# Performance work log

Hardware: AMD Instinct MI355X
Metric: run time of the kernel (lower is better)

## Reference

```python
import jax, jax.numpy as jnp
import numpy as np

B = 8192
TEXT_DIM = 2048
GRAPH_DIM = 1024
OUT_DIM = 1024
C = 2048  # common_dim = max(text_dim, graph_dim)
H = 16    # num_heads
LN_EPS = 1e-5


def _linear(x, W, b):
    # torch nn.Linear: y = x @ W.T + b, W: [out, in]
    return x @ W.T + b


def _mha(q, k, v, Wqkv, bqkv, Wo, bo):
    # Faithful to torch nn.MultiheadAttention (batch_first, eval mode).
    # Wqkv: [3C, C], bqkv: [3C], Wo: [C, C], bo: [C]
    Bq, S, _ = q.shape
    D = C // H
    Wq, Wk, Wv = Wqkv[:C], Wqkv[C:2 * C], Wqkv[2 * C:]
    bq, bk, bv = bqkv[:C], bqkv[C:2 * C], bqkv[2 * C:]
    qh = _linear(q, Wq, bq).reshape(Bq, S, H, D).transpose(0, 2, 1, 3)  # [B,H,S,D]
    kh = _linear(k, Wk, bk).reshape(Bq, S, H, D).transpose(0, 2, 1, 3)
    vh = _linear(v, Wv, bv).reshape(Bq, S, H, D).transpose(0, 2, 1, 3)
    scores = jnp.einsum('bhqd,bhkd->bhqk', qh, kh) / jnp.sqrt(jnp.asarray(D, qh.dtype))
    attn = jax.nn.softmax(scores, axis=-1)
    out = jnp.einsum('bhqk,bhkd->bhqd', attn, vh)
    out = out.transpose(0, 2, 1, 3).reshape(Bq, S, C)
    return _linear(out, Wo, bo)


def _layernorm(x, w, b):
    mu = jnp.mean(x, axis=-1, keepdims=True)
    var = jnp.mean(jnp.square(x - mu), axis=-1, keepdims=True)
    return (x - mu) * jax.lax.rsqrt(var + LN_EPS) * w + b


def setup_inputs() -> dict:
    key = jax.random.key(0)
    ks = jax.random.split(key, 16)
    s = 0.02
    return {
        'text_embeddings': jax.random.normal(ks[0], (B, TEXT_DIM), jnp.float32),
        'graph_embeddings': jax.random.normal(ks[1], (B, GRAPH_DIM), jnp.float32),
        'Wt': jax.random.normal(ks[2], (C, TEXT_DIM), jnp.float32) * s,
        'bt': jnp.zeros((C,), jnp.float32),
        'Wg': jax.random.normal(ks[3], (C, GRAPH_DIM), jnp.float32) * s,
        'bg': jnp.zeros((C,), jnp.float32),
        'Wqkv_s': jax.random.normal(ks[4], (3 * C, C), jnp.float32) * s,
        'bqkv_s': jnp.zeros((3 * C,), jnp.float32),
        'Wo_s': jax.random.normal(ks[5], (C, C), jnp.float32) * s,
        'bo_s': jnp.zeros((C,), jnp.float32),
        'Wqkv_c': jax.random.normal(ks[6], (3 * C, C), jnp.float32) * s,
        'bqkv_c': jnp.zeros((3 * C,), jnp.float32),
        'Wo_c': jax.random.normal(ks[7], (C, C), jnp.float32) * s,
        'bo_c': jnp.zeros((C,), jnp.float32),
        'ln_w': jnp.ones((C,), jnp.float32),
        'ln_b': jnp.zeros((C,), jnp.float32),
        'Wout': jax.random.normal(ks[8], (OUT_DIM, C), jnp.float32) * s,
        'bout': jnp.zeros((OUT_DIM,), jnp.float32),
    }


def reference(text_embeddings, graph_embeddings, Wt, bt, Wg, bg,
              Wqkv_s, bqkv_s, Wo_s, bo_s, Wqkv_c, bqkv_c, Wo_c, bo_c,
              ln_w, ln_b, Wout, bout):
    text_proj = _linear(text_embeddings, Wt, bt)    # [B, C]
    graph_proj = _linear(graph_embeddings, Wg, bg)  # [B, C]
    stacked = jnp.stack([text_proj, graph_proj], axis=1)  # [B, 2, C]
    attn_out = _mha(stacked, stacked, stacked, Wqkv_s, bqkv_s, Wo_s, bo_s)
    attn_out = _layernorm(attn_out, ln_w, ln_b)
    cross = _mha(attn_out, stacked, stacked, Wqkv_c, bqkv_c, Wo_c, bo_c)
    attn_out = attn_out + cross
    fused = jnp.mean(attn_out, axis=1)  # [B, C]
    return _linear(fused, Wout, bout)   # [B, OUT_DIM]
```

## Files before the change

### kernel.cpp

```cpp
#include <hip/hip_runtime.h>
#include <cstdio>

typedef unsigned short u16;
typedef float f32x4 __attribute__((ext_vector_type(4)));
typedef short s16x8 __attribute__((ext_vector_type(8)));

__device__ __forceinline__ u16 f2bf(float x) {
    unsigned u = __float_as_uint(x);
    u += 0x7fffu + ((u >> 16) & 1u);
    return (u16)(u >> 16);
}
__device__ __forceinline__ unsigned pack2(float a, float b) {
    return (unsigned)f2bf(a) | ((unsigned)f2bf(b) << 16);
}
__device__ __forceinline__ void unpack2(unsigned u, float& lo, float& hi) {
    lo = __uint_as_float(u << 16);
    hi = __uint_as_float(u & 0xffff0000u);
}

__device__ __forceinline__ void gl2lds16(const u16* g, u16* l) {
    __builtin_amdgcn_global_load_lds(
        (const __attribute__((address_space(1))) void*)g,
        (__attribute__((address_space(3))) void*)l, 16, 0, 0);
}

__global__ __launch_bounds__(256) void cast_w7(
    const float* __restrict__ p0, const float* __restrict__ p1,
    const float* __restrict__ p2, const float* __restrict__ p3,
    const float* __restrict__ p4, const float* __restrict__ p5,
    const float* __restrict__ p6, u16* __restrict__ dst) {
    long i = (long)blockIdx.x * 256 + threadIdx.x;
    if (i >= 10485760L) return;
    const float* src;
    long base;
    if (i < 3145728L)      { src = p0; base = 0L; }
    else if (i < 6291456L) { src = p1; base = 3145728L; }
    else if (i < 7340032L) { src = p2; base = 6291456L; }
    else if (i < 8388608L) { src = p3; base = 7340032L; }
    else if (i < 9437184L) { src = p4; base = 8388608L; }
    else if (i < 9961472L) { src = p5; base = 9437184L; }
    else                   { src = p6; base = 9961472L; }
    float4 v = ((const float4*)src)[i - base];
    uint2 r;
    r.x = pack2(v.x, v.y);
    r.y = pack2(v.z, v.w);
    ((uint2*)dst)[i] = r;
}

__global__ __launch_bounds__(256) void cast_in(const float* __restrict__ t,
                                               const float* __restrict__ g,
                                               u16* __restrict__ yt,
                                               u16* __restrict__ yg,
                                               int nt4, int ng4) {
    int i = blockIdx.x * 256 + threadIdx.x;
    const float* src;
    u16* dst;
    int idx;
    if (i < nt4) {
        src = t; dst = yt; idx = i;
    } else {
        idx = i - nt4;
        if (idx >= ng4) return;
        src = g; dst = yg;
    }
    float4 v = ((const float4*)src)[idx];
    uint2 r;
    r.x = pack2(v.x, v.y);
    r.y = pack2(v.z, v.w);
    ((uint2*)dst)[idx] = r;
}

template <bool OUT_BF16>
__global__ __launch_bounds__(256) void gemm_async(const u16* __restrict__ A, int lda,
                                                  const u16* __restrict__ B,
                                                  const float* __restrict__ bias,
                                                  void* __restrict__ Cout,
                                                  int K, int ldc) {
    __shared__ __align__(16) u16 As[128 * 32];
    __shared__ __align__(16) u16 Bs[128 * 32];

    const int tid = threadIdx.x;
    const int lane = tid & 63;
    const int wave = tid >> 6;
    const int wm = wave >> 1;
    const int wn = wave & 1;
    const size_t bm = (size_t)blockIdx.y * 128;
    const size_t bn = (size_t)blockIdx.x * 128;

    f32x4 acc[4][4];
#pragma unroll
    for (int i = 0; i < 4; ++i)
#pragma unroll
        for (int j = 0; j < 4; ++j) acc[i][j] = (f32x4)0.f;

    const int srow = tid >> 2;
    const int scol = (tid & 3) << 3;
    const u16* Ag = A + (bm + (size_t)srow) * (size_t)lda + scol;
    const u16* Bg = B + (bn + (size_t)srow) * (size_t)K + scol;
    const size_t rA = (size_t)64 * lda;
    const size_t rB = (size_t)64 * K;
    u16* lA0 = &As[tid * 8];
    u16* lA1 = &As[2048 + tid * 8];
    u16* lB0 = &Bs[tid * 8];
    u16* lB1 = &Bs[2048 + tid * 8];

    const int lrow = lane & 15;
    const int lk = (lane >> 4) << 3;

    const int niter = K >> 5;
    for (int t = 0; t < niter; ++t) {
        __syncthreads();
        gl2lds16(Ag, lA0);
        gl2lds16(Ag + rA, lA1);
        gl2lds16(Bg, lB0);
        gl2lds16(Bg + rB, lB1);
        Ag += 32;
        Bg += 32;
        __syncthreads();
        s16x8 af[4], bfr[4];
#pragma unroll
        for (int i = 0; i < 4; ++i)
            af[i] = *(const s16x8*)&As[(wm * 64 + i * 16 + lrow) * 32 + lk];
#pragma unroll
        for (int j = 0; j < 4; ++j)
            bfr[j] = *(const s16x8*)&Bs[(wn * 64 + j * 16 + lrow) * 32 + lk];
#pragma unroll
        for (int i = 0; i < 4; ++i)
#pragma unroll
            for (int j = 0; j < 4; ++j)
                acc[i][j] = __builtin_amdgcn_mfma_f32_16x16x32_bf16(
                    af[i], bfr[j], acc[i][j], 0, 0, 0);
    }

    const size_t crow0 = bm + wm * 64 + ((lane >> 4) << 2);
    const int ccol0 = (int)bn + wn * 64 + (lane & 15);
#pragma unroll
    for (int i = 0; i < 4; ++i) {
#pragma unroll
        for (int j = 0; j < 4; ++j) {
            const int col = ccol0 + j * 16;
            const float bv = bias[col];
            const size_t base = (crow0 + (size_t)i * 16) * (size_t)ldc + col;
#pragma unroll
            for (int r = 0; r < 4; ++r) {
                const float v = acc[i][j][r] + bv;
                if (OUT_BF16)
                    ((u16*)Cout)[base + (size_t)r * ldc] = f2bf(v);
                else
                    ((float*)Cout)[base + (size_t)r * ldc] = v;
            }
        }
    }
}

#define STG_A02(v)                                                            \
    do {                                                                      \
        gl2lds16(aG + (size_t)(v) * 64, &As[(v) & 1][tid * 8]);               \
        gl2lds16(aG + 2 * a64 + (size_t)(v) * 64,                             \
                 &As[(v) & 1][8192 + tid * 8]);                               \
    } while (0)
#define STG_A13(v)                                                            \
    do {                                                                      \
        gl2lds16(aG + a64 + (size_t)(v) * 64, &As[(v) & 1][4096 + tid * 8]);  \
        gl2lds16(aG + 3 * a64 + (size_t)(v) * 64,                             \
                 &As[(v) & 1][12288 + tid * 8]);                              \
    } while (0)
#define STG_B01(v)                                                            \
    do {                                                                      \
        gl2lds16(bG + (size_t)(v) * 64, &Bs[(v) & 1][tid * 8]);               \
        gl2lds16(bG + b64 + (size_t)(v) * 64, &Bs[(v) & 1][4096 + tid * 8]);  \
    } while (0)
#define STG_B23(v)                                                            \
    do {                                                                      \
        gl2lds16(bG + 2 * b64 + (size_t)(v) * 64,                             \
                 &Bs[(v) & 1][8192 + tid * 8]);                               \
        gl2lds16(bG + 3 * b64 + (size_t)(v) * 64,                             \
                 &Bs[(v) & 1][12288 + tid * 8]);                              \
    } while (0)
#define RD_AF(buf, mh, m)                                                     \
    do {                                                                      \
        const u16* p_ = &As[buf][aRow + ((mh) * 64 + (m) * 16) * 64];         \
        aF[m][0] = *(const s16x8*)(p_ + aK0);                                 \
        aF[m][1] = *(const s16x8*)(p_ + aK1);                                 \
    } while (0)
#define RD_B(buf, nh, dst)                                                    \
    do {                                                                      \
        _Pragma("unroll") for (int n_ = 0; n_ < 2; ++n_) {                    \
            const u16* p_ = &Bs[buf][bRow + ((nh) * 32 + n_ * 16) * 64];      \
            dst[n_][0] = *(const s16x8*)(p_ + aK0);                           \
            dst[n_][1] = *(const s16x8*)(p_ + aK1);                           \
        }                                                                     \
    } while (0)
#define MFMA4(ar, bv, ci, cj)                                                 \
    do {                                                                      \
        acc[ci][cj] = __builtin_amdgcn_mfma_f32_16x16x32_bf16(                \
            (ar)[0], (bv)[0], acc[ci][cj], 0, 0, 0);                          \
        acc[ci][cj] = __builtin_amdgcn_mfma_f32_16x16x32_bf16(                \
            (ar)[1], (bv)[1], acc[ci][cj], 0, 0, 0);                          \
    } while (0)

#define TILEW(u, SA13, S2, RDN, V2S, V4S)                                     \
    do {                                                                      \
        const int cur = (u) & 1, oth = cur ^ 1;                               \
                                                          \
        if (SA13) STG_A13((u) + 1);                                           \
        RD_B(cur, 1, b1);                                                     \
        __builtin_amdgcn_s_setprio(1);                                        \
        _Pragma("unroll") for (int m = 0; m < 4; ++m) {                       \
            MFMA4(aF[m], b0[0], m, 0);                                        \
            MFMA4(aF[m], b0[1], m, 1);                                        \
        }                                                                     \
        __builtin_amdgcn_s_setprio(0);                                        \
        asm volatile("s_waitcnt " V2S ::: "memory");                          \
        __builtin_amdgcn_s_barrier();                                         \
                                  \
        if (S2) STG_A02((u) + 2);                                             \
        __builtin_amdgcn_s_setprio(1);                                        \
        _Pragma("unroll") for (int m = 0; m < 4; ++m) {                       \
            MFMA4(aF[m], b1[0], m, 2);                                        \
            MFMA4(aF[m], b1[1], m, 3);                                        \
            RD_AF(cur, 1, m);                                                 \
        }                                                                     \
        __builtin_amdgcn_s_setprio(0);                                        \
        __builtin_amdgcn_s_barrier();                                         \
                                                          \
        if (S2) STG_B01((u) + 2);                                             \
        __builtin_amdgcn_s_setprio(1);                                        \
        _Pragma("unroll") for (int m = 0; m < 4; ++m) {                       \
            MFMA4(aF[m], b1[0], 4 + m, 2);                                    \
            MFMA4(aF[m], b1[1], 4 + m, 3);                                    \
        }                                                                     \
        __builtin_amdgcn_s_setprio(0);                                        \
        asm volatile("s_waitcnt " V4S ::: "memory");                          \
        __builtin_amdgcn_s_barrier();                                         \
                         \
        if (S2) STG_B23((u) + 2);                                             \
        __builtin_amdgcn_s_setprio(1);                                        \
        _Pragma("unroll") for (int m = 0; m < 4; ++m) {                       \
            MFMA4(aF[m], b0[0], 4 + m, 0);                                    \
            MFMA4(aF[m], b0[1], 4 + m, 1);                                    \
            if (RDN) RD_AF(oth, 0, m);                                        \
        }                                                                     \
        __builtin_amdgcn_s_setprio(0);                                        \
        if (RDN) RD_B(oth, 0, b0);                                            \
        __builtin_amdgcn_s_barrier();                                         \
    } while (0)

template <bool OUT_BF16>
__global__ __launch_bounds__(512, 2) void gemm8(const u16* __restrict__ A, int lda,
                                                const u16* __restrict__ B,
                                                const float* __restrict__ bias,
                                                void* __restrict__ Cout,
                                                int K, int ldc) {
    __shared__ __align__(16) u16 As[2][16384];
    __shared__ __align__(16) u16 Bs[2][16384];

    const int tid = threadIdx.x;
    const int lane = tid & 63;
    const int wave = tid >> 6;
    const int wm = wave >> 2;
    const int wn = wave & 3;

    const unsigned nwg = gridDim.x * gridDim.y;
    const unsigned orig = blockIdx.y * gridDim.x + blockIdx.x;
    const unsigned q = nwg >> 3, r = nwg & 7u;
    const unsigned xcd = orig & 7u, idx = orig >> 3;
    const unsigned wg =
        (xcd < r ? xcd * (q + 1) : r * (q + 1) + (xcd - r) * q) + idx;
    const size_t bm = (size_t)(wg / gridDim.x) * 256;
    const size_t bn = (size_t)(wg % gridDim.x) * 256;

    f32x4 acc[8][4];
#pragma unroll
    for (int i = 0; i < 8; ++i)
#pragma unroll
        for (int j = 0; j < 4; ++j) acc[i][j] = (f32x4)0.f;

    const int strow = tid >> 3;
    const int ssw = ((tid & 7) << 3) ^ ((strow & 7) << 3);
    const u16* aG = A + (bm + (size_t)strow) * (size_t)lda + ssw;
    const u16* bG = B + (bn + (size_t)strow) * (size_t)K + ssw;
    const size_t a64 = (size_t)64 * lda;
    const size_t b64 = (size_t)64 * K;

    const int lrow = lane & 15;
    const int hi8 = (lane >> 4) << 3;
    const int fswz = (lrow & 7) << 3;
    const int aK0 = hi8 ^ fswz;
    const int aK1 = (32 + hi8) ^ fswz;
    const int aRow = (wm * 128 + lrow) * 64;
    const int bRow = (wn * 64 + lrow) * 64;

    s16x8 aF[4][2], b0[2][2], b1[2][2];

    const int NT = K >> 6;

    STG_A02(0);
    STG_A13(0);
    STG_B01(0);
    STG_B23(0);
    STG_A02(1);
    STG_B01(1);
    STG_B23(1);
    asm volatile("s_waitcnt vmcnt(6)" ::: "memory");
    __builtin_amdgcn_s_barrier();
#pragma unroll
    for (int m = 0; m < 4; ++m) RD_AF(0, 0, m);
    RD_B(0, 0, b0);

    for (int u = 0; u < NT - 2; ++u)
        TILEW(u, 1, 1, 1, "vmcnt(8)", "vmcnt(6)");
    TILEW(NT - 2, 1, 0, 1, "vmcnt(8)", "vmcnt(2)");
    TILEW(NT - 1, 0, 0, 0, "vmcnt(0)", "vmcnt(0)");

    const size_t crow0 = bm + wm * 128 + ((lane >> 4) << 2);
    const int ccol0 = (int)bn + wn * 64 + (lane & 15);
#pragma unroll
    for (int im = 0; im < 8; ++im) {
#pragma unroll
        for (int in = 0; in < 4; ++in) {
            const int col = ccol0 + in * 16;
            const float bv = bias[col];
            const size_t base = (crow0 + (size_t)im * 16) * (size_t)ldc + col;
#pragma unroll
            for (int r = 0; r < 4; ++r) {
                const float v = acc[im][in][r] + bv;
                if (OUT_BF16)
                    ((u16*)Cout)[base + (size_t)r * ldc] = f2bf(v);
                else
                    ((float*)Cout)[base + (size_t)r * ldc] = v;
            }
        }
    }
}

#undef STG_A02
#undef STG_A13
#undef STG_B01
#undef STG_B23
#undef RD_AF
#undef RD_B
#undef MFMA4
#undef TILEW

__device__ __forceinline__ void dot8(uint4 a, uint4 b, float& acc) {
    const unsigned* pa = (const unsigned*)&a;
    const unsigned* pb = (const unsigned*)&b;
#pragma unroll
    for (int i = 0; i < 4; ++i) {
        float alo, ahi, blo, bhi;
        unpack2(pa[i], alo, ahi);
        unpack2(pb[i], blo, bhi);
        acc += alo * blo + ahi * bhi;
    }
}

__global__ __launch_bounds__(256) void attn2(u16* __restrict__ qkv) {
    const int b = (blockIdx.x * 256 + threadIdx.x) >> 6;
    const int l = threadIdx.x & 63;
    u16* t0 = qkv + (size_t)(2 * b) * 6144;
    u16* t1 = t0 + 6144;
    const float scale = 0.0883883476483184f;
#pragma unroll
    for (int hg = 0; hg < 4; ++hg) {
        const int o = hg * 512 + l * 8;
        const uint4 q0 = *(const uint4*)(t0 + o);
        const uint4 q1 = *(const uint4*)(t1 + o);
        const uint4 k0 = *(const uint4*)(t0 + 2048 + o);
        const uint4 k1 = *(const uint4*)(t1 + 2048 + o);
        float s00 = 0.f, s01 = 0.f, s10 = 0.f, s11 = 0.f;
        dot8(q0, k0, s00);
        dot8(q0, k1, s01);
        dot8(q1, k0, s10);
        dot8(q1, k1, s11);
#pragma unroll
        for (int m = 1; m < 16; m <<= 1) {
            s00 += __shfl_xor(s00, m);
            s01 += __shfl_xor(s01, m);
            s10 += __shfl_xor(s10, m);
            s11 += __shfl_xor(s11, m);
        }
        s00 *= scale; s01 *= scale; s10 *= scale; s11 *= scale;
        const float m0 = fmaxf(s00, s01), m1 = fmaxf(s10, s11);
        const float e00 = __expf(s00 - m0), e01 = __expf(s01 - m0);
        const float e10 = __expf(s10 - m1), e11 = __expf(s11 - m1);
        const float r0 = 1.f / (e00 + e01), r1 = 1.f / (e10 + e11);
        const float p00 = e00 * r0, p01 = e01 * r0;
        const float p10 = e10 * r1, p11 = e11 * r1;
        const uint4 v0 = *(const uint4*)(t0 + 4096 + o);
        const uint4 v1 = *(const uint4*)(t1 + 4096 + o);
        const unsigned* pv0 = (const unsigned*)&v0;
        const unsigned* pv1 = (const unsigned*)&v1;
        uint4 c0v, c1v;
        unsigned* pc0 = (unsigned*)&c0v;
        unsigned* pc1 = (unsigned*)&c1v;
#pragma unroll
        for (int i = 0; i < 4; ++i) {
            float alo, ahi, blo, bhi;
            unpack2(pv0[i], alo, ahi);
            unpack2(pv1[i], blo, bhi);
            pc0[i] = pack2(p00 * alo + p01 * blo, p00 * ahi + p01 * bhi);
            pc1[i] = pack2(p10 * alo + p11 * blo, p10 * ahi + p11 * bhi);
        }
        *(uint4*)(t0 + o) = c0v;
        *(uint4*)(t1 + o) = c1v;
    }
}

__global__ __launch_bounds__(256) void ln_k(const u16* __restrict__ x, int ldx,
                                            const float* __restrict__ w,
                                            const float* __restrict__ bb,
                                            u16* __restrict__ y) {
    __shared__ float red[8];
    const int row = blockIdx.x;
    const int tid = threadIdx.x;
    const uint4 v = ((const uint4*)(x + (size_t)row * ldx))[tid];
    const unsigned* pw = (const unsigned*)&v;
    float f[8];
#pragma unroll
    for (int i = 0; i < 4; ++i) unpack2(pw[i], f[2 * i], f[2 * i + 1]);
    float s = 0.f, q = 0.f;
#pragma unroll
    for (int i = 0; i < 8; ++i) {
        s += f[i];
        q += f[i] * f[i];
    }
#pragma unroll
    for (int off = 32; off > 0; off >>= 1) {
        s += __shfl_down(s, off);
        q += __shfl_down(q, off);
    }
    if ((tid & 63) == 0) {
        red[tid >> 6] = s;
        red[4 + (tid >> 6)] = q;
    }
    __syncthreads();
    s = red[0] + red[1] + red[2] + red[3];
    q = red[4] + red[5] + red[6] + red[7];
    const float mu = s * (1.f / 2048.f);
    const float var = q * (1.f / 2048.f) - mu * mu;
    const float rstd = rsqrtf(var + 1e-5f);
    const float4 w0 = ((const float4*)w)[2 * tid];
    const float4 w1 = ((const float4*)w)[2 * tid + 1];
    const float4 b0 = ((const float4*)bb)[2 * tid];
    const float4 b1 = ((const float4*)bb)[2 * tid + 1];
    const float wv[8] = {w0.x, w0.y, w0.z, w0.w, w1.x, w1.y, w1.z, w1.w};
    const float bv[8] = {b0.x, b0.y, b0.z, b0.w, b1.x, b1.y, b1.z, b1.w};
    uint4 o;
    unsigned* po = (unsigned*)&o;
#pragma unroll
    for (int i = 0; i < 4; ++i) {
        float lo = (f[2 * i] - mu) * rstd * wv[2 * i] + bv[2 * i];
        float hi = (f[2 * i + 1] - mu) * rstd * wv[2 * i + 1] + bv[2 * i + 1];
        po[i] = pack2(lo, hi);
    }
    ((uint4*)(y + (size_t)row * 2048))[tid] = o;
}

__global__ __launch_bounds__(256) void mean_res(const u16* __restrict__ ln,
                                                const u16* __restrict__ co,
                                                u16* __restrict__ fused) {
    const int gid = blockIdx.x * 256 + threadIdx.x;
    const int b = gid >> 8;
    const int c8 = gid & 255;
    const uint4 l0 = ((const uint4*)(ln + (size_t)(2 * b) * 2048))[c8];
    const uint4 l1 = ((const uint4*)(ln + (size_t)(2 * b + 1) * 2048))[c8];
    const uint4 c0 = ((const uint4*)(co + (size_t)(2 * b) * 6144))[c8];
    const uint4 c1 = ((const uint4*)(co + (size_t)(2 * b + 1) * 6144))[c8];
    const unsigned* pl0 = (const unsigned*)&l0;
    const unsigned* pl1 = (const unsigned*)&l1;
    const unsigned* pc0 = (const unsigned*)&c0;
    const unsigned* pc1 = (const unsigned*)&c1;
    uint4 o;
    unsigned* po = (unsigned*)&o;
#pragma unroll
    for (int i = 0; i < 4; ++i) {
        float a_lo, a_hi, b_lo, b_hi, c_lo, c_hi, d_lo, d_hi;
        unpack2(pl0[i], a_lo, a_hi);
        unpack2(pl1[i], b_lo, b_hi);
        unpack2(pc0[i], c_lo, c_hi);
        unpack2(pc1[i], d_lo, d_hi);
        po[i] = pack2(0.5f * (a_lo + c_lo + b_lo + d_lo),
                      0.5f * (a_hi + c_hi + b_hi + d_hi));
    }
    ((uint4*)(fused + (size_t)b * 12288))[c8] = o;
}

extern "C" void kernel_launch(void* const* d_in, const int* in_sizes, int n_in,
                              void* d_out, int out_size, void* d_ws, size_t ws_size,
                              hipStream_t stream) {
    (void)in_sizes; (void)n_in; (void)out_size;
    const float* text   = (const float*)d_in[0];
    const float* graph  = (const float*)d_in[1];
    const float* Wt     = (const float*)d_in[2];
    const float* bt     = (const float*)d_in[3];
    const float* Wg     = (const float*)d_in[4];
    const float* bg     = (const float*)d_in[5];
    const float* Wqkv_s = (const float*)d_in[6];
    const float* bqkv_s = (const float*)d_in[7];
    const float* Wo_s   = (const float*)d_in[8];
    const float* bo_s   = (const float*)d_in[9];
    const float* Wqkv_c = (const float*)d_in[10];
    const float* bqkv_c = (const float*)d_in[11];
    const float* Wo_c   = (const float*)d_in[12];
    const float* bo_c   = (const float*)d_in[13];
    const float* ln_w   = (const float*)d_in[14];
    const float* ln_b   = (const float*)d_in[15];
    const float* Wout   = (const float*)d_in[16];
    const float* bout   = (const float*)d_in[17];
    float* out = (float*)d_out;

    char* ws = (char*)d_ws;
    u16* wQs  = (u16*)ws;
    u16* wQc  = wQs + 12582912ull;
    u16* wOs  = wQc + 12582912ull;
    u16* wOc  = wOs + 4194304ull;
    u16* wWt  = wOc + 4194304ull;
    u16* wWg  = wWt + 4194304ull;
    u16* wOut = wWg + 2097152ull;
    const size_t WB = 83886080ull;

    size_t CH = 8192;
    while (CH > 256 && WB + 40960ull * CH > ws_size) CH >>= 1;
    fprintf(stderr, "[kernel_launch] ws_size=%zu need=%zu CH=%zu\n",
            ws_size, WB + 40960ull * CH, CH);
    if (WB + 40960ull * CH > ws_size || d_ws == nullptr) return;

    const size_t T = 2 * CH;
    char* ca = ws + WB;
    u16* stacked_c = (u16*)ca;
    u16* ln_c      = (u16*)(ca + 4096 * T);
    u16* qkv_c     = (u16*)(ca + 8192 * T);
    u16* tb_c = qkv_c;
    u16* gb_c = qkv_c + (size_t)CH * 2048;

    cast_w7<<<40960, 256, 0, stream>>>(Wqkv_s, Wqkv_c, Wo_s, Wo_c, Wt, Wg,
                                       Wout, wQs);

    const dim3 blk(256);
    const dim3 blk8(512);
    const unsigned gy  = (unsigned)(CH / 128);
    const unsigned gy8 = (unsigned)(CH / 256);
    const unsigned g8  = (unsigned)(T / 256);

    for (size_t c0 = 0; c0 < 8192; c0 += CH) {
        {
            const int nt4 = (int)(CH * 512);
            const int ng4 = (int)(CH * 256);
            cast_in<<<(unsigned)((nt4 + ng4 + 255) / 256), blk, 0, stream>>>(
                text + c0 * 2048, graph + c0 * 1024, tb_c, gb_c, nt4, ng4);
        }
        gemm8<true><<<dim3(8, gy8), blk8, 0, stream>>>(
            tb_c, 2048, wWt, bt, stacked_c, 2048, 4096);
        gemm8<true><<<dim3(8, gy8), blk8, 0, stream>>>(
            gb_c, 1024, wWg, bg, stacked_c + 2048, 1024, 4096);
        gemm8<true><<<dim3(24, g8), blk8, 0, stream>>>(
            stacked_c, 2048, wQs, bqkv_s, qkv_c, 2048, 6144);
        attn2<<<(unsigned)(CH / 4), blk, 0, stream>>>(qkv_c);
        gemm8<true><<<dim3(8, g8), blk8, 0, stream>>>(
            qkv_c, 6144, wOs, bo_s, qkv_c + 4096, 2048, 6144);
        ln_k<<<(unsigned)T, blk, 0, stream>>>(qkv_c + 4096, 6144, ln_w, ln_b, ln_c);
        gemm8<true><<<dim3(8, g8), blk8, 0, stream>>>(
            ln_c, 2048, wQc, bqkv_c, qkv_c, 2048, 6144);
        gemm8<true><<<dim3(16, g8), blk8, 0, stream>>>(
            stacked_c, 2048, wQc + 2048ull * 2048, bqkv_c + 2048,
            qkv_c + 2048, 2048, 6144);
        attn2<<<(unsigned)(CH / 4), blk, 0, stream>>>(qkv_c);
        gemm8<true><<<dim3(8, g8), blk8, 0, stream>>>(
            qkv_c, 6144, wOc, bo_c, qkv_c + 4096, 2048, 6144);
        mean_res<<<(unsigned)CH, blk, 0, stream>>>(ln_c, qkv_c + 4096, qkv_c);
        gemm_async<false><<<dim3(8, gy), blk, 0, stream>>>(
            qkv_c, 12288, wOut, bout, out + c0 * 1024, 2048, 1024);
    }
}
```

Baseline: 1.797 ms.

## Switch GEMM to single-buffered LDS with in-place staged refills

Replaces the 256x256 GEMM's double-buffered LDS tiles with one buffer per operand. Each quarter of the next K-tile is now loaded into a region as soon as the waves have finished reading it. The B rows are remapped in LDS so that the regions each wave consumes first can be overwritten early. This halves LDS use, which may allow more workgroups per CU, but the prefetch distance drops from two tiles to one and the loop waits on vmcnt(0) more often, so latency hiding could get worse.

```diff
diff --git a/kernel.cpp b/kernel.cpp
--- a/kernel.cpp
+++ b/kernel.cpp
@@ -155,38 +155,34 @@
 
 #define STG_A02(v)                                                            \
     do {                                                                      \
-        gl2lds16(aG + (size_t)(v) * 64, &As[(v) & 1][tid * 8]);               \
-        gl2lds16(aG + 2 * a64 + (size_t)(v) * 64,                             \
-                 &As[(v) & 1][8192 + tid * 8]);                               \
+        gl2lds16(aG + (size_t)(v) * 64, &As[tid * 8]);                        \
+        gl2lds16(aG + 2 * a64 + (size_t)(v) * 64, &As[8192 + tid * 8]);       \
     } while (0)
 #define STG_A13(v)                                                            \
     do {                                                                      \
-        gl2lds16(aG + a64 + (size_t)(v) * 64, &As[(v) & 1][4096 + tid * 8]);  \
-        gl2lds16(aG + 3 * a64 + (size_t)(v) * 64,                             \
-                 &As[(v) & 1][12288 + tid * 8]);                              \
-    } while (0)
-#define STG_B01(v)                                                            \
-    do {                                                                      \
-        gl2lds16(bG + (size_t)(v) * 64, &Bs[(v) & 1][tid * 8]);               \
-        gl2lds16(bG + b64 + (size_t)(v) * 64, &Bs[(v) & 1][4096 + tid * 8]);  \
-    } while (0)
-#define STG_B23(v)                                                            \
-    do {                                                                      \
-        gl2lds16(bG + 2 * b64 + (size_t)(v) * 64,                             \
-                 &Bs[(v) & 1][8192 + tid * 8]);                               \
-        gl2lds16(bG + 3 * b64 + (size_t)(v) * 64,                             \
-                 &Bs[(v) & 1][12288 + tid * 8]);                              \
-    } while (0)
-#define RD_AF(buf, mh, m)                                                     \
-    do {                                                                      \
-        const u16* p_ = &As[buf][aRow + ((mh) * 64 + (m) * 16) * 64];         \
+        gl2lds16(aG + a64 + (size_t)(v) * 64, &As[4096 + tid * 8]);           \
+        gl2lds16(aG + 3 * a64 + (size_t)(v) * 64, &As[12288 + tid * 8]);      \
+    } while (0)
+#define STG_B0(v)                                                             \
+    do {                                                                      \
+        gl2lds16(bG + (size_t)(v) * 64, &Bs[tid * 8]);                        \
+        gl2lds16(bG + 128 * bK + (size_t)(v) * 64, &Bs[4096 + tid * 8]);      \
+    } while (0)
+#define STG_B1(v)                                                             \
+    do {                                                                      \
+        gl2lds16(bG + 32 * bK + (size_t)(v) * 64, &Bs[8192 + tid * 8]);       \
+        gl2lds16(bG + 160 * bK + (size_t)(v) * 64, &Bs[12288 + tid * 8]);     \
+    } while (0)
+#define RD_AF(mh, m)                                                          \
+    do {                                                                      \
+        const u16* p_ = &As[aRow + ((mh) * 64 + (m) * 16) * 64];              \
         aF[m][0] = *(const s16x8*)(p_ + aK0);                                 \
         aF[m][1] = *(const s16x8*)(p_ + aK1);                                 \
     } while (0)
-#define RD_B(buf, nh, dst)                                                    \
+#define RD_B(nh, dst)                                                         \
     do {                                                                      \
         _Pragma("unroll") for (int n_ = 0; n_ < 2; ++n_) {                    \
-            const u16* p_ = &Bs[buf][bRow + ((nh) * 32 + n_ * 16) * 64];      \
+            const u16* p_ = &Bs[bRowL + ((nh) * 128 + n_ * 16) * 64];         \
             dst[n_][0] = *(const s16x8*)(p_ + aK0);                           \
             dst[n_][1] = *(const s16x8*)(p_ + aK1);                           \
         }                                                                     \
@@ -199,50 +195,49 @@
             (ar)[1], (bv)[1], acc[ci][cj], 0, 0, 0);                          \
     } while (0)
 
-#define TILEW(u, SA13, S2, RDN, V2S, V4S)                                     \
-    do {                                                                      \
-        const int cur = (u) & 1, oth = cur ^ 1;                               \
+#define TILE1(u, S, RDN, W3S, W4S)                                            \
+    do {                                                                      \
                                                           \
-        if (SA13) STG_A13((u) + 1);                                           \
-        RD_B(cur, 1, b1);                                                     \
+        RD_B(1, b1);                                                          \
         __builtin_amdgcn_s_setprio(1);                                        \
         _Pragma("unroll") for (int m = 0; m < 4; ++m) {                       \
             MFMA4(aF[m], b0[0], m, 0);                                        \
             MFMA4(aF[m], b0[1], m, 1);                                        \
         }                                                                     \
         __builtin_amdgcn_s_setprio(0);                                        \
-        asm volatile("s_waitcnt " V2S ::: "memory");                          \
+        asm volatile("s_waitcnt vmcnt(0)" ::: "memory");                      \
         __builtin_amdgcn_s_barrier();                                         \
-                                  \
-        if (S2) STG_A02((u) + 2);                                             \
+                                    \
+        if (S) { STG_A02((u) + 1); STG_B0((u) + 1); }                         \
         __builtin_amdgcn_s_setprio(1);                                        \
         _Pragma("unroll") for (int m = 0; m < 4; ++m) {                       \
             MFMA4(aF[m], b1[0], m, 2);                                        \
             MFMA4(aF[m], b1[1], m, 3);                                        \
-            RD_AF(cur, 1, m);                                                 \
+            RD_AF(1, m);                                                      \
         }                                                                     \
         __builtin_amdgcn_s_setprio(0);                                        \
         __builtin_amdgcn_s_barrier();                                         \
                                                           \
-        if (S2) STG_B01((u) + 2);                                             \
+        if (S) STG_B1((u) + 1);                                               \
         __builtin_amdgcn_s_setprio(1);                                        \
         _Pragma("unroll") for (int m = 0; m < 4; ++m) {                       \
             MFMA4(aF[m], b1[0], 4 + m, 2);                                    \
             MFMA4(aF[m], b1[1], 4 + m, 3);                                    \
         }                                                                     \
         __builtin_amdgcn_s_setprio(0);                                        \
-        asm volatile("s_waitcnt " V4S ::: "memory");                          \
+        asm volatile("s_waitcnt " W3S ::: "memory");                          \
         __builtin_amdgcn_s_barrier();                                         \
-                         \
-        if (S2) STG_B23((u) + 2);                                             \
+                     \
+        if (S) STG_A13((u) + 1);                                              \
         __builtin_amdgcn_s_setprio(1);                                        \
         _Pragma("unroll") for (int m = 0; m < 4; ++m) {                       \
             MFMA4(aF[m], b0[0], 4 + m, 0);                                    \
             MFMA4(aF[m], b0[1], 4 + m, 1);                                    \
-            if (RDN) RD_AF(oth, 0, m);                                        \
+            if (RDN) RD_AF(0, m);                                             \
         }                                                                     \
         __builtin_amdgcn_s_setprio(0);                                        \
-        if (RDN) RD_B(oth, 0, b0);                                            \
+        if (RDN) RD_B(0, b0);                                                 \
+        asm volatile("s_waitcnt " W4S ::: "memory");                          \
         __builtin_amdgcn_s_barrier();                                         \
     } while (0)
 
@@ -252,8 +247,8 @@
                                                 const float* __restrict__ bias,
                                                 void* __restrict__ Cout,
                                                 int K, int ldc) {
-    __shared__ __align__(16) u16 As[2][16384];
-    __shared__ __align__(16) u16 Bs[2][16384];
+    __shared__ __align__(16) u16 As[16384];
+    __shared__ __align__(16) u16 Bs[16384];
 
     const int tid = threadIdx.x;
     const int lane = tid & 63;
@@ -279,9 +274,10 @@
     const int strow = tid >> 3;
     const int ssw = ((tid & 7) << 3) ^ ((strow & 7) << 3);
     const u16* aG = A + (bm + (size_t)strow) * (size_t)lda + ssw;
-    const u16* bG = B + (bn + (size_t)strow) * (size_t)K + ssw;
     const size_t a64 = (size_t)64 * lda;
-    const size_t b64 = (size_t)64 * K;
+    const size_t bK = (size_t)K;
+    const u16* bG =
+        B + (bn + (size_t)((strow >> 5) * 64 + (strow & 31))) * bK + ssw;
 
     const int lrow = lane & 15;
     const int hi8 = (lane >> 4) << 3;
@@ -289,7 +285,7 @@
     const int aK0 = hi8 ^ fswz;
     const int aK1 = (32 + hi8) ^ fswz;
     const int aRow = (wm * 128 + lrow) * 64;
-    const int bRow = (wn * 64 + lrow) * 64;
+    const int bRowL = (((wn >> 1) << 6) + ((wn & 1) << 5) + lrow) * 64;
 
     s16x8 aF[4][2], b0[2][2], b1[2][2];
 
@@ -297,21 +293,17 @@
 
     STG_A02(0);
     STG_A13(0);
-    STG_B01(0);
-    STG_B23(0);
-    STG_A02(1);
-    STG_B01(1);
-    STG_B23(1);
-    asm volatile("s_waitcnt vmcnt(6)" ::: "memory");
+    STG_B0(0);
+    STG_B1(0);
+    asm volatile("s_waitcnt vmcnt(0)" ::: "memory");
     __builtin_amdgcn_s_barrier();
 #pragma unroll
-    for (int m = 0; m < 4; ++m) RD_AF(0, 0, m);
-    RD_B(0, 0, b0);
-
-    for (int u = 0; u < NT - 2; ++u)
-        TILEW(u, 1, 1, 1, "vmcnt(8)", "vmcnt(6)");
-    TILEW(NT - 2, 1, 0, 1, "vmcnt(8)", "vmcnt(2)");
-    TILEW(NT - 1, 0, 0, 0, "vmcnt(0)", "vmcnt(0)");
+    for (int m = 0; m < 4; ++m) RD_AF(0, m);
+    RD_B(0, b0);
+
+    for (int u = 0; u < NT - 1; ++u)
+        TILE1(u, 1, 1, "vmcnt(2)", "vmcnt(2)");
+    TILE1(NT - 1, 0, 0, "vmcnt(0)", "vmcnt(0)");
 
     const size_t crow0 = bm + wm * 128 + ((lane >> 4) << 2);
     const int ccol0 = (int)bn + wn * 64 + (lane & 15);
@@ -336,12 +328,12 @@
 
 #undef STG_A02
 #undef STG_A13
-#undef STG_B01
-#undef STG_B23
+#undef STG_B0
+#undef STG_B1
 #undef RD_AF
 #undef RD_B
 #undef MFMA4
-#undef TILEW
+#undef TILE1
 
 __device__ __forceinline__ void dot8(uint4 a, uint4 b, float& acc) {
     const unsigned* pa = (const unsigned*)&a;
```

After: 1.849 ms. 1.03x slower.
